# Kernel optimization log

Hardware: AMD Instinct MI355X
Metric: run time of the kernel (lower is better)

## Reference

```python
import jax, jax.numpy as jnp
import numpy as np

IN_F = 4096
OUT_F = 4096
B, S = 2, 2048


def setup_inputs() -> dict:
    key = jax.random.key(0)
    k1, k2, k3, k4 = jax.random.split(key, 4)
    input = jax.random.normal(k1, (B, S, IN_F), dtype=jnp.float32)
    int8_weights = jax.random.randint(k2, (OUT_F, IN_F), -128, 128, dtype=jnp.int32).astype(jnp.int8)
    scales = jax.random.normal(k3, (OUT_F,), dtype=jnp.float32)
    bias = jax.random.normal(k4, (1, OUT_F), dtype=jnp.float32)
    return {"input": input, "int8_weights": int8_weights, "scales": scales, "bias": bias}


def reference(input, int8_weights, scales, bias):
    # F.linear(x, W) = x @ W.T ; dequant via per-output-channel scale, then bias
    w = int8_weights.astype(input.dtype)          # [out, in]
    out = jnp.einsum('bsi,oi->bso', input, w)     # [B, S, out]
    out = out * scales + bias                      # broadcast [out] and [1, out]
    return out
```

## Files before the change

### kernel.cpp

```cpp
#include <hip/hip_runtime.h>
#include <hip/hip_bf16.h>

typedef unsigned short u16;
typedef unsigned int u32;
typedef unsigned char u8;
typedef __attribute__((ext_vector_type(4))) int i32x4;

#define MM 4096
#define NN 4096
#define KK 4096

#define BAR __builtin_amdgcn_s_barrier()
#define FENCE asm volatile("" ::: "memory")
#define WAITVM(n) asm volatile("s_waitcnt vmcnt(" #n ")" ::: "memory")

#define ABUF(sh, b) ((sh) + (b) * 65536)
#define BBUF(sh, b) ((sh) + 32768 + (b) * 65536)

__global__ __launch_bounds__(256) void cvt_k(const int* __restrict__ w,
                                             u8* __restrict__ ow,
                                             const float* __restrict__ x,
                                             u8* __restrict__ oa,
                                             float* __restrict__ dA) {
  const int bid = blockIdx.x;
  const int t = threadIdx.x;
  if (bid < 4096) {
    int i = bid * 256 + t;
    const int4* w4 = (const int4*)w + (size_t)i * 4;
    i32x4 r;
#pragma unroll
    for (int j = 0; j < 4; ++j) {
      int4 v = w4[j];
      r[j] = (v.x & 255) | ((v.y & 255) << 8) | ((v.z & 255) << 16) |
             ((u32)(v.w & 255) << 24);
    }
    *(i32x4*)(ow + (size_t)i * 16) = r;
  } else {
    const int row = bid - 4096;
    const float4* xr = (const float4*)(x + (size_t)row * KK);
    float4 v[4];
    float mx = 0.f;
#pragma unroll
    for (int j = 0; j < 4; ++j) {
      v[j] = xr[t + j * 256];
      mx = fmaxf(mx, fmaxf(fmaxf(fabsf(v[j].x), fabsf(v[j].y)),
                           fmaxf(fabsf(v[j].z), fabsf(v[j].w))));
    }
#pragma unroll
    for (int off = 32; off; off >>= 1) mx = fmaxf(mx, __shfl_down(mx, off));
    __shared__ float sm[4];
    if ((t & 63) == 0) sm[t >> 6] = mx;
    __syncthreads();
    mx = fmaxf(fmaxf(sm[0], sm[1]), fmaxf(sm[2], sm[3]));
    mx = fmaxf(mx, 1e-20f);
    const float inv = 127.0f / mx;
    if (t == 0) dA[row] = mx / 127.0f;
    u32* orow = (u32*)(oa + (size_t)row * KK);
#pragma unroll
    for (int j = 0; j < 4; ++j) {
      int qx = (int)rintf(v[j].x * inv), qy = (int)rintf(v[j].y * inv);
      int qz = (int)rintf(v[j].z * inv), qw = (int)rintf(v[j].w * inv);
      orow[t + j * 256] =
          (qx & 255) | ((qy & 255) << 8) | ((qz & 255) << 16) | ((u32)(qw & 255) << 24);
    }
  }
}

__device__ __forceinline__ void gload16(const u8* g, u8* l) {
  __builtin_amdgcn_global_load_lds(
      (const __attribute__((address_space(1))) void*)g,
      (__attribute__((address_space(3))) void*)l, 16, 0, 0);
}

__device__ __forceinline__ void stage_q(const u8* __restrict__ gRowBase,
                                        int k0, u8* lds, int tid, int pass) {
  int p = pass * 512 + tid;
  int row = p >> 3;
  int c = (p & 7) ^ (row & 7);
  gload16(gRowBase + (size_t)row * KK + k0 + c * 16, lds + p * 16);
}

__device__ __forceinline__ i32x4 ldsfrag(const u8* base, int r, int q) {
  return *(const i32x4*)(base + r * 128 + (((q ^ r) & 7) << 4));
}

#define MFMAI8(a, b, c) __builtin_amdgcn_mfma_i32_16x16x64_i8(a, b, c, 0, 0, 0)

template <bool LAST>
__device__ __forceinline__ void do_tile(
    int t, i32x4 (&acc)[8][4], const u8* Ag, const u8* Wg, u8* sh,
    int tid, int lr, int hi, int wr, int wc,
    i32x4 (&afr0)[4], i32x4 (&afr1)[4], i32x4 (&b01)[2], i32x4 (&b23)[2]) {
  const int b = t & 1;
  u8* Acur = ABUF(sh, b);
  u8* Anxt = ABUF(sh, b ^ 1);
  u8* Bcur = BBUF(sh, b);
  u8* Bnxt = BBUF(sh, b ^ 1);

#pragma unroll
  for (int n = 0; n < 2; ++n)
    b23[n] = ldsfrag(Bcur, wc * 64 + (2 + n) * 16 + lr, hi);
  if (!LAST) {
#pragma unroll
    for (int ps = 0; ps < 4; ++ps) stage_q(Wg, (t + 1) * 128, Bnxt, tid, ps);
  }
  __builtin_amdgcn_s_setprio(1);
#pragma unroll
  for (int m = 0; m < 4; ++m)
#pragma unroll
    for (int n = 0; n < 2; ++n)
      acc[m][n] = MFMAI8(afr0[m], b01[n], acc[m][n]);
  __builtin_amdgcn_s_setprio(0);

#pragma unroll
  for (int m = 0; m < 4; ++m)
    afr1[m] = ldsfrag(Acur, wr * 128 + 64 + m * 16 + lr, hi);
  if (!LAST) {
#pragma unroll
    for (int ps = 0; ps < 4; ++ps) stage_q(Ag, (t + 1) * 128, Anxt, tid, ps);
  }
  __builtin_amdgcn_s_setprio(1);
#pragma unroll
  for (int m = 0; m < 4; ++m)
#pragma unroll
    for (int n = 0; n < 2; ++n)
      acc[m][2 + n] = MFMAI8(afr0[m], b23[n], acc[m][2 + n]);
  __builtin_amdgcn_s_setprio(0);

#pragma unroll
  for (int m = 0; m < 4; ++m)
    afr0[m] = ldsfrag(Acur, wr * 128 + m * 16 + lr, 4 + hi);
  __builtin_amdgcn_s_setprio(1);
#pragma unroll
  for (int m = 0; m < 4; ++m)
#pragma unroll
    for (int n = 0; n < 2; ++n)
      acc[4 + m][n] = MFMAI8(afr1[m], b01[n], acc[4 + m][n]);
  __builtin_amdgcn_s_setprio(0);

#pragma unroll
  for (int n = 0; n < 2; ++n)
    b01[n] = ldsfrag(Bcur, wc * 64 + n * 16 + lr, 4 + hi);
  __builtin_amdgcn_s_setprio(1);
#pragma unroll
  for (int m = 0; m < 4; ++m)
#pragma unroll
    for (int n = 0; n < 2; ++n)
      acc[4 + m][2 + n] = MFMAI8(afr1[m], b23[n], acc[4 + m][2 + n]);
  __builtin_amdgcn_s_setprio(0);

#pragma unroll
  for (int n = 0; n < 2; ++n)
    b23[n] = ldsfrag(Bcur, wc * 64 + (2 + n) * 16 + lr, 4 + hi);
  __builtin_amdgcn_s_setprio(1);
#pragma unroll
  for (int m = 0; m < 4; ++m)
#pragma unroll
    for (int n = 0; n < 2; ++n)
      acc[m][n] = MFMAI8(afr0[m], b01[n], acc[m][n]);
  __builtin_amdgcn_s_setprio(0);

#pragma unroll
  for (int m = 0; m < 4; ++m)
    afr1[m] = ldsfrag(Acur, wr * 128 + 64 + m * 16 + lr, 4 + hi);
  __builtin_amdgcn_s_setprio(1);
#pragma unroll
  for (int m = 0; m < 4; ++m)
#pragma unroll
    for (int n = 0; n < 2; ++n)
      acc[m][2 + n] = MFMAI8(afr0[m], b23[n], acc[m][2 + n]);
  __builtin_amdgcn_s_setprio(0);
  if (!LAST) {
    WAITVM(0);
    FENCE; BAR;
  }

  if (!LAST) {
#pragma unroll
    for (int m = 0; m < 4; ++m)
      afr0[m] = ldsfrag(Anxt, wr * 128 + m * 16 + lr, hi);
  }
  __builtin_amdgcn_s_setprio(1);
#pragma unroll
  for (int m = 0; m < 4; ++m)
#pragma unroll
    for (int n = 0; n < 2; ++n)
      acc[4 + m][n] = MFMAI8(afr1[m], b01[n], acc[4 + m][n]);
  __builtin_amdgcn_s_setprio(0);

  if (!LAST) {
#pragma unroll
    for (int n = 0; n < 2; ++n)
      b01[n] = ldsfrag(Bnxt, wc * 64 + n * 16 + lr, hi);
  }
  __builtin_amdgcn_s_setprio(1);
#pragma unroll
  for (int m = 0; m < 4; ++m)
#pragma unroll
    for (int n = 0; n < 2; ++n)
      acc[4 + m][2 + n] = MFMAI8(afr1[m], b23[n], acc[4 + m][2 + n]);
  __builtin_amdgcn_s_setprio(0);
}

__global__ __launch_bounds__(512, 2) void gemm_k(const u8* __restrict__ A,
                                                 const u8* __restrict__ W,
                                                 const float* __restrict__ dA,
                                                 const float* __restrict__ scales,
                                                 const float* __restrict__ bias,
                                                 float* __restrict__ out) {
  __shared__ u8 sh[131072];

  const int cpx = gridDim.x >> 3;
  const int wg = (blockIdx.x & 7) * cpx + (blockIdx.x >> 3);
  const int bm = wg >> 4;
  const int bn = wg & 15;

  const int tid = threadIdx.x;
  const int lane = tid & 63;
  const int lr = lane & 15;
  const int hi = lane >> 4;
  const int wid = tid >> 6;
  const int wr = wid >> 2;
  const int wc = wid & 3;

  i32x4 acc[8][4] = {};
  i32x4 afr0[4], afr1[4], b01[2], b23[2];

  const u8* Ag = A + (size_t)bm * 256 * KK;
  const u8* Wg = W + (size_t)bn * 256 * KK;

#pragma unroll
  for (int ps = 0; ps < 4; ++ps) stage_q(Wg, 0, BBUF(sh, 0), tid, ps);
#pragma unroll
  for (int ps = 0; ps < 4; ++ps) stage_q(Ag, 0, ABUF(sh, 0), tid, ps);
  WAITVM(0);
  FENCE; BAR;
#pragma unroll
  for (int m = 0; m < 4; ++m)
    afr0[m] = ldsfrag(ABUF(sh, 0), wr * 128 + m * 16 + lr, hi);
#pragma unroll
  for (int n = 0; n < 2; ++n)
    b01[n] = ldsfrag(BBUF(sh, 0), wc * 64 + n * 16 + lr, hi);

  for (int t = 0; t < 31; ++t)
    do_tile<false>(t, acc, Ag, Wg, sh, tid, lr, hi, wr, wc, afr0, afr1, b01, b23);
  do_tile<true>(31, acc, Ag, Wg, sh, tid, lr, hi, wr, wc, afr0, afr1, b01, b23);

  const int colb = bn * 256 + wc * 64 + lr;
  const int rowb0 = bm * 256 + wr * 128 + (hi << 2);
#pragma unroll
  for (int m = 0; m < 8; ++m) {
    const int row = rowb0 + m * 16;
    const float da0 = dA[row], da1 = dA[row + 1], da2 = dA[row + 2], da3 = dA[row + 3];
#pragma unroll
    for (int n = 0; n < 4; ++n) {
      const int col = colb + n * 16;
      const float sc = scales[col];
      const float bi = bias[col];
      out[(size_t)(row + 0) * NN + col] = (float)acc[m][n][0] * (da0 * sc) + bi;
      out[(size_t)(row + 1) * NN + col] = (float)acc[m][n][1] * (da1 * sc) + bi;
      out[(size_t)(row + 2) * NN + col] = (float)acc[m][n][2] * (da2 * sc) + bi;
      out[(size_t)(row + 3) * NN + col] = (float)acc[m][n][3] * (da3 * sc) + bi;
    }
  }
}

__global__ __launch_bounds__(256) void fb_k(const float* __restrict__ A,
                                            const int* __restrict__ W,
                                            const float* __restrict__ scales,
                                            const float* __restrict__ bias,
                                            float* __restrict__ out) {
  __shared__ float Arow[KK];
  const int m = blockIdx.y;
  const int n0 = blockIdx.x * 256;
  const int tid = threadIdx.x;
  for (int k = tid; k < KK; k += 256) Arow[k] = A[(size_t)m * KK + k];
  __syncthreads();
  const int n = n0 + tid;
  float acc = 0.f;
  const int* wrp = W + (size_t)n * KK;
  for (int k = 0; k < KK; ++k) acc += Arow[k] * (float)wrp[k];
  out[(size_t)m * NN + n] = acc * scales[n] + bias[n];
}

extern "C" void kernel_launch(void* const* d_in, const int* in_sizes, int n_in,
                              void* d_out, int out_size, void* d_ws, size_t ws_size,
                              hipStream_t stream) {
  const float* input = (const float*)d_in[0];
  const int* w8 = (const int*)d_in[1];
  const float* scales = (const float*)d_in[2];
  const float* bias = (const float*)d_in[3];
  float* out = (float*)d_out;

  const size_t nelem = (size_t)NN * KK;
  const size_t need = 2 * nelem + MM * sizeof(float);

  if (ws_size >= need) {
    u8* Wq = (u8*)d_ws;
    u8* Aq = Wq + nelem;
    float* dA = (float*)(Aq + nelem);
    cvt_k<<<8192, 256, 0, stream>>>(w8, Wq, input, Aq, dA);
    gemm_k<<<256, 512, 0, stream>>>(Aq, Wq, dA, scales, bias, out);
  } else {
    dim3 grid(NN / 256, MM);
    fb_k<<<grid, 256, 0, stream>>>(input, w8, scales, bias, out);
  }
}
```

Baseline: 90.28 us.

## Store LDS tiles in MFMA fragment order so reads are contiguous per lane

```diff
diff --git a/kernel.cpp b/kernel.cpp
--- a/kernel.cpp
+++ b/kernel.cpp
@@ -14,8 +14,8 @@
 #define FENCE asm volatile("" ::: "memory")
 #define WAITVM(n) asm volatile("s_waitcnt vmcnt(" #n ")" ::: "memory")
 
-#define ABUF(sh, b) ((sh) + (b) * 65536)
-#define BBUF(sh, b) ((sh) + 32768 + (b) * 65536)
+#define ABUFO(b) ((b) * 32768)
+#define BBUFO(b) (65536 + (b) * 32768)
 
 __global__ __launch_bounds__(256) void cvt_k(const int* __restrict__ w,
                                              u8* __restrict__ ow,
@@ -72,16 +72,16 @@
       (__attribute__((address_space(3))) void*)l, 16, 0, 0);
 }
 
-__device__ __forceinline__ void stage_q(const u8* __restrict__ gRowBase,
-                                        int k0, u8* lds, int tid, int pass) {
-  int p = pass * 512 + tid;
-  int row = p >> 3;
-  int c = (p & 7) ^ (row & 7);
-  gload16(gRowBase + (size_t)row * KK + k0 + c * 16, lds + p * 16);
-}
-
-__device__ __forceinline__ i32x4 ldsfrag(const u8* base, int r, int q) {
-  return *(const i32x4*)(base + r * 128 + (((q ^ r) & 7) << 4));
+__device__ __forceinline__ void stage_frag(const u8* __restrict__ gRowBase,
+                                           int k0, u8* sh, int tileOff, int f,
+                                           int lr, int hi, int lane16) {
+  gload16(gRowBase + (size_t)((f >> 1) * 16 + lr) * KK + k0 + (f & 1) * 64 + hi * 16,
+          sh + tileOff + f * 1024 + lane16);
+}
+
+__device__ __forceinline__ i32x4 ldsfrag(const u8* sh, int tileOff, int g,
+                                         int kh, int lane16) {
+  return *(const i32x4*)(sh + tileOff + (g * 2 + kh) * 1024 + lane16);
 }
 
 #define MFMAI8(a, b, c) __builtin_amdgcn_mfma_i32_16x16x64_i8(a, b, c, 0, 0, 0)
@@ -89,20 +89,21 @@
 template <bool LAST>
 __device__ __forceinline__ void do_tile(
     int t, i32x4 (&acc)[8][4], const u8* Ag, const u8* Wg, u8* sh,
-    int tid, int lr, int hi, int wr, int wc,
+    int wid, int lr, int hi, int lane16, int wr, int wc,
     i32x4 (&afr0)[4], i32x4 (&afr1)[4], i32x4 (&b01)[2], i32x4 (&b23)[2]) {
   const int b = t & 1;
-  u8* Acur = ABUF(sh, b);
-  u8* Anxt = ABUF(sh, b ^ 1);
-  u8* Bcur = BBUF(sh, b);
-  u8* Bnxt = BBUF(sh, b ^ 1);
+  const int Ac = ABUFO(b), An = ABUFO(b ^ 1);
+  const int Bc = BBUFO(b), Bn = BBUFO(b ^ 1);
+  const int ga = wr * 8;
+  const int gb = wc * 4;
 
 #pragma unroll
   for (int n = 0; n < 2; ++n)
-    b23[n] = ldsfrag(Bcur, wc * 64 + (2 + n) * 16 + lr, hi);
-  if (!LAST) {
-#pragma unroll
-    for (int ps = 0; ps < 4; ++ps) stage_q(Wg, (t + 1) * 128, Bnxt, tid, ps);
+    b23[n] = ldsfrag(sh, Bc, gb + 2 + n, 0, lane16);
+  if (!LAST) {
+#pragma unroll
+    for (int i = 0; i < 4; ++i)
+      stage_frag(Wg, (t + 1) * 128, sh, Bn, i * 8 + wid, lr, hi, lane16);
   }
   __builtin_amdgcn_s_setprio(1);
 #pragma unroll
@@ -114,10 +115,11 @@
 
 #pragma unroll
   for (int m = 0; m < 4; ++m)
-    afr1[m] = ldsfrag(Acur, wr * 128 + 64 + m * 16 + lr, hi);
-  if (!LAST) {
-#pragma unroll
-    for (int ps = 0; ps < 4; ++ps) stage_q(Ag, (t + 1) * 128, Anxt, tid, ps);
+    afr1[m] = ldsfrag(sh, Ac, ga + 4 + m, 0, lane16);
+  if (!LAST) {
+#pragma unroll
+    for (int i = 0; i < 4; ++i)
+      stage_frag(Ag, (t + 1) * 128, sh, An, i * 8 + wid, lr, hi, lane16);
   }
   __builtin_amdgcn_s_setprio(1);
 #pragma unroll
@@ -129,7 +131,7 @@
 
 #pragma unroll
   for (int m = 0; m < 4; ++m)
-    afr0[m] = ldsfrag(Acur, wr * 128 + m * 16 + lr, 4 + hi);
+    afr0[m] = ldsfrag(sh, Ac, ga + m, 1, lane16);
   __builtin_amdgcn_s_setprio(1);
 #pragma unroll
   for (int m = 0; m < 4; ++m)
@@ -140,7 +142,7 @@
 
 #pragma unroll
   for (int n = 0; n < 2; ++n)
-    b01[n] = ldsfrag(Bcur, wc * 64 + n * 16 + lr, 4 + hi);
+    b01[n] = ldsfrag(sh, Bc, gb + n, 1, lane16);
   __builtin_amdgcn_s_setprio(1);
 #pragma unroll
   for (int m = 0; m < 4; ++m)
@@ -151,7 +153,7 @@
 
 #pragma unroll
   for (int n = 0; n < 2; ++n)
-    b23[n] = ldsfrag(Bcur, wc * 64 + (2 + n) * 16 + lr, 4 + hi);
+    b23[n] = ldsfrag(sh, Bc, gb + 2 + n, 1, lane16);
   __builtin_amdgcn_s_setprio(1);
 #pragma unroll
   for (int m = 0; m < 4; ++m)
@@ -162,7 +164,7 @@
 
 #pragma unroll
   for (int m = 0; m < 4; ++m)
-    afr1[m] = ldsfrag(Acur, wr * 128 + 64 + m * 16 + lr, 4 + hi);
+    afr1[m] = ldsfrag(sh, Ac, ga + 4 + m, 1, lane16);
   __builtin_amdgcn_s_setprio(1);
 #pragma unroll
   for (int m = 0; m < 4; ++m)
@@ -178,7 +180,7 @@
   if (!LAST) {
 #pragma unroll
     for (int m = 0; m < 4; ++m)
-      afr0[m] = ldsfrag(Anxt, wr * 128 + m * 16 + lr, hi);
+      afr0[m] = ldsfrag(sh, An, ga + m, 0, lane16);
   }
   __builtin_amdgcn_s_setprio(1);
 #pragma unroll
@@ -191,7 +193,7 @@
   if (!LAST) {
 #pragma unroll
     for (int n = 0; n < 2; ++n)
-      b01[n] = ldsfrag(Bnxt, wc * 64 + n * 16 + lr, hi);
+      b01[n] = ldsfrag(sh, Bn, gb + n, 0, lane16);
   }
   __builtin_amdgcn_s_setprio(1);
 #pragma unroll
@@ -219,6 +221,7 @@
   const int lane = tid & 63;
   const int lr = lane & 15;
   const int hi = lane >> 4;
+  const int lane16 = lane * 16;
   const int wid = tid >> 6;
   const int wr = wid >> 2;
   const int wc = wid & 3;
@@ -230,21 +233,25 @@
   const u8* Wg = W + (size_t)bn * 256 * KK;
 
 #pragma unroll
-  for (int ps = 0; ps < 4; ++ps) stage_q(Wg, 0, BBUF(sh, 0), tid, ps);
-#pragma unroll
-  for (int ps = 0; ps < 4; ++ps) stage_q(Ag, 0, ABUF(sh, 0), tid, ps);
+  for (int i = 0; i < 4; ++i)
+    stage_frag(Wg, 0, sh, BBUFO(0), i * 8 + wid, lr, hi, lane16);
+#pragma unroll
+  for (int i = 0; i < 4; ++i)
+    stage_frag(Ag, 0, sh, ABUFO(0), i * 8 + wid, lr, hi, lane16);
   WAITVM(0);
   FENCE; BAR;
 #pragma unroll
   for (int m = 0; m < 4; ++m)
-    afr0[m] = ldsfrag(ABUF(sh, 0), wr * 128 + m * 16 + lr, hi);
+    afr0[m] = ldsfrag(sh, ABUFO(0), wr * 8 + m, 0, lane16);
 #pragma unroll
   for (int n = 0; n < 2; ++n)
-    b01[n] = ldsfrag(BBUF(sh, 0), wc * 64 + n * 16 + lr, hi);
+    b01[n] = ldsfrag(sh, BBUFO(0), wc * 4 + n, 0, lane16);
 
   for (int t = 0; t < 31; ++t)
-    do_tile<false>(t, acc, Ag, Wg, sh, tid, lr, hi, wr, wc, afr0, afr1, b01, b23);
-  do_tile<true>(31, acc, Ag, Wg, sh, tid, lr, hi, wr, wc, afr0, afr1, b01, b23);
+    do_tile<false>(t, acc, Ag, Wg, sh, wid, lr, hi, lane16, wr, wc,
+                   afr0, afr1, b01, b23);
+  do_tile<true>(31, acc, Ag, Wg, sh, wid, lr, hi, lane16, wr, wc,
+                afr0, afr1, b01, b23);
 
   const int colb = bn * 256 + wc * 64 + lr;
   const int rowb0 = bm * 256 + wr * 128 + (hi << 2);
```

After: 114.6 us. 26.9% more time.
